# Optimization experiments

Hardware: AMD Instinct MI355X
Metric: run time of the kernel (lower is better)

Reference implementation:

```python
import jax, jax.numpy as jnp
import numpy as np

EPS = 1e-5  # BatchNorm eps


def _mlp(x, w1, b1, w2, b2, g, bt):
    # NRI MLP: elu(fc1) -> elu(fc2) -> batchnorm over all leading dims (training-mode batch stats)
    h = jax.nn.elu(x @ w1.T + b1)
    h = jax.nn.elu(h @ w2.T + b2)
    f = h.reshape(-1, h.shape[-1])
    mu = f.mean(0)
    var = f.var(0)  # biased, as in torch BN normalization
    return (h - mu) * jax.lax.rsqrt(var + EPS) * g + bt


def _gru(x, w_ih, w_hh, b_ih, b_hh):
    # x: [B, T, D] batch_first; torch GRU gate order (r, z, n)
    gi = jnp.einsum('btd,hd->bth', x, w_ih) + b_ih  # precompute input gates
    H = w_hh.shape[1]
    h0 = jnp.zeros((x.shape[0], H), x.dtype)

    def step(h, gi_t):
        gh = h @ w_hh.T + b_hh
        ir, iz, inn = jnp.split(gi_t, 3, -1)
        hr, hz, hn = jnp.split(gh, 3, -1)
        r = jax.nn.sigmoid(ir + hr)
        z = jax.nn.sigmoid(iz + hz)
        n = jnp.tanh(inn + r * hn)
        h_new = (1.0 - z) * n + z * h
        return h_new, h_new

    hT, ys = jax.lax.scan(step, h0, gi.transpose(1, 0, 2))
    return ys.transpose(1, 0, 2), hT


def _xavier(key, shape):
    std = np.sqrt(2.0 / (shape[0] + shape[1])).astype(np.float32)
    return jax.random.normal(key, shape, jnp.float32) * std


def setup_inputs() -> dict:
    key = jax.random.key(0)
    ks = iter(jax.random.split(key, 64))
    B, N, T, Fin, H, O = 8, 30, 100, 4, 128, 2
    inputs = jax.random.normal(next(ks), (B, N, T, Fin), jnp.float32)
    r, s = np.nonzero(1 - np.eye(N))  # fully connected, no self loops -> E = N*(N-1)
    eye = np.eye(N, dtype=np.float32)
    d = {
        'inputs': inputs,
        'rel_rec': jnp.asarray(eye[r]),
        'rel_send': jnp.asarray(eye[s]),
    }
    dims = {1: Fin, 2: 2 * H, 3: H, 4: 3 * H}
    for k in (1, 2, 3, 4):
        d[f'm{k}_w1'] = _xavier(next(ks), (H, dims[k]))
        d[f'm{k}_b1'] = jnp.full((H,), 0.1, jnp.float32)
        d[f'm{k}_w2'] = _xavier(next(ks), (H, H))
        d[f'm{k}_b2'] = jnp.full((H,), 0.1, jnp.float32)
        d[f'm{k}_g'] = jnp.ones((H,), jnp.float32)
        d[f'm{k}_bt'] = jnp.zeros((H,), jnp.float32)
    u = float(1.0 / np.sqrt(H))
    for p in ('gf', 'gr'):
        d[f'{p}_wih'] = jax.random.uniform(next(ks), (3 * H, H), jnp.float32, -u, u)
        d[f'{p}_whh'] = jax.random.uniform(next(ks), (3 * H, H), jnp.float32, -u, u)
        d[f'{p}_bih'] = jax.random.uniform(next(ks), (3 * H,), jnp.float32, -u, u)
        d[f'{p}_bhh'] = jax.random.uniform(next(ks), (3 * H,), jnp.float32, -u, u)
    d['pw'] = _xavier(next(ks), (O, H))
    d['pb'] = jnp.full((O,), 0.1, jnp.float32)
    d['ew'] = _xavier(next(ks), (O, 2 * H))
    d['eb'] = jnp.full((O,), 0.1, jnp.float32)
    return d


def reference(inputs, rel_rec, rel_send, m1_w1, m1_b1, m1_w2, m1_b2, m1_g, m1_bt, m2_w1, m2_b1, m2_w2, m2_b2, m2_g, m2_bt, m3_w1, m3_b1, m3_w2, m3_b2, m3_g, m3_bt, m4_w1, m4_b1, m4_w2, m4_b2, m4_g, m4_bt, gf_wih, gf_whh, gf_bih, gf_bhh, gr_wih, gr_whh, gr_bih, gr_bhh, pw, pb, ew, eb):
    N = rel_rec.shape[1]

    def node2edge(x):  # x: [B,N,T,H] -> [B,E,T,2H]
        snd = jnp.einsum('en,bnth->beth', rel_send, x)
        rcv = jnp.einsum('en,bnth->beth', rel_rec, x)
        return jnp.concatenate([snd, rcv], -1)

    def edge2node(x):  # x: [B,E,T,H] -> [B,N,T,H], mean-style normalization by N
        return jnp.einsum('en,beth->bnth', rel_rec, x) / N

    x = _mlp(inputs, m1_w1, m1_b1, m1_w2, m1_b2, m1_g, m1_bt)      # [B,N,T,H]
    x = node2edge(x)                                                # [B,E,T,2H]
    x = _mlp(x, m2_w1, m2_b1, m2_w2, m2_b2, m2_g, m2_bt)            # [B,E,T,H]
    x_skip = x
    x = edge2node(x)                                                # [B,N,T,H]
    x = _mlp(x, m3_w1, m3_b1, m3_w2, m3_b2, m3_g, m3_bt)
    x = node2edge(x)                                                # [B,E,T,2H]
    x = jnp.concatenate([x, x_skip], -1)                            # [B,E,T,3H]
    x = _mlp(x, m4_w1, m4_b1, m4_w2, m4_b2, m4_g, m4_bt)            # [B,E,T,H]

    B, E, T, H = x.shape
    xr = x.reshape(B * E, T, H)
    fwd_x, hT = _gru(xr, gf_wih, gf_whh, gf_bih, gf_bhh)
    rev_x, _ = _gru(xr[:, ::-1], gr_wih, gr_whh, gr_bih, gr_bhh)
    rev_x = rev_x[:, ::-1]

    prior = (fwd_x @ pw.T + pb).reshape(B, E, T, -1)
    comb = jnp.concatenate([fwd_x, rev_x], -1)
    enc = (comb @ ew.T + eb).reshape(B, E, T, -1)
    return prior, enc, hT[None]  # hT[None] matches torch GRU h_n [1, B*E, H]
```

## Files before the change

### kernel.cpp

```cpp
#include <hip/hip_runtime.h>
#include <math.h>

typedef float f32x4 __attribute__((ext_vector_type(4)));
typedef short bf16x8 __attribute__((ext_vector_type(8)));
typedef unsigned int uint32;
#define DEV static __device__ __forceinline__

constexpr int B_ = 8, N_ = 30, T_ = 100, FIN = 4, H_ = 128;
constexpr int E_ = N_*(N_-1);
constexpr int NSEQ = B_*E_;
constexpr int RN = B_*N_*T_;
constexpr int RE = B_*E_*T_;
constexpr int ET = E_*T_;
constexpr int NB_GRU = (NSEQ + 63)/64;

DEV float eluf(float x){ return x > 0.f ? x : __expf(x) - 1.f; }
DEV float sigmoidf(float x){ return 1.f/(1.f + __expf(-x)); }
DEV float tanhfast(float x){
  float cx = fminf(fmaxf(x, -20.f), 20.f);
  float e = __expf(2.f*cx);
  return (e - 1.f)/(e + 1.f);
}
DEV float dot4(f32x4 a, f32x4 b){ return a[0]*b[0] + a[1]*b[1] + a[2]*b[2] + a[3]*b[3]; }

DEV float bf2f(unsigned short u){ return __uint_as_float(((uint32)u) << 16); }
DEV uint32 f2bf_bits(float f){ uint32 b = __float_as_uint(f); return (b + 0x7FFFu + ((b >> 16) & 1u)) >> 16; }
DEV uint32 pack2(float lo, float hi){ return f2bf_bits(lo) | (f2bf_bits(hi) << 16); }

DEV bf16x8 cvt8(const float* __restrict__ p){
  f32x4 a = *(const f32x4*)p;
  f32x4 b = *(const f32x4*)(p+4);
  bf16x8 r;
  r[0]=(short)f2bf_bits(a[0]); r[1]=(short)f2bf_bits(a[1]);
  r[2]=(short)f2bf_bits(a[2]); r[3]=(short)f2bf_bits(a[3]);
  r[4]=(short)f2bf_bits(b[0]); r[5]=(short)f2bf_bits(b[1]);
  r[6]=(short)f2bf_bits(b[2]); r[7]=(short)f2bf_bits(b[3]);
  return r;
}

DEV void edge_decomp(int row, int& b, int& t, int& sn, int& ir)
{
  b = row / ET;
  int rem = row - b*ET;
  int e   = rem / T_;
  t = rem - e*T_;
  ir = e / (N_-1);
  int j = e - ir*(N_-1);
  sn = j + (j >= ir ? 1 : 0);
}

DEV int xcd_swizzle(int orig, int nwg)
{
  int q = nwg >> 3, r = nwg & 7;
  int xcd = orig & 7, j = orig >> 3;
  return (xcd < r ? xcd*(q+1) : r*(q+1) + (xcd-r)*q) + j;
}

__global__ __launch_bounds__(256)
void prep_weights(const float* __restrict__ w21, const float* __restrict__ w22,
                  const float* __restrict__ w41, const float* __restrict__ w42,
                  unsigned short* __restrict__ wbf)
{
  int idx = blockIdx.x*256 + threadIdx.x;
  if (idx >= 114688) return;
  float v;
  if (idx < 32768)      v = w21[idx];
  else if (idx < 49152) v = w22[idx - 32768];
  else if (idx < 98304) v = w41[idx - 49152];
  else                  v = w42[idx - 98304];
  wbf[idx] = (unsigned short)f2bf_bits(v);
}

template<int MODE, int DIN>
__global__ __launch_bounds__(256)
void mlp_fused(const float* __restrict__ src,
               const float* __restrict__ w1, const float* __restrict__ b1,
               const float* __restrict__ w2, const float* __restrict__ b2,
               float* __restrict__ out)
{
  constexpr int KC  = (DIN < 32) ? DIN : 32;
  constexpr int NCH = DIN / KC;
  __shared__ float As[KC][68];
  __shared__ float Ws[32][132];
  __shared__ float Hs[128][68];

  const int tid  = threadIdx.x;
  const int row0 = blockIdx.x * 64;
  const int tx = tid & 15, ty = tid >> 4;
  const int c0 = tx*8, r0 = ty*4;

  float acc[4][8];
  #pragma unroll
  for (int j=0;j<4;++j){
    #pragma unroll
    for (int i=0;i<8;++i) acc[j][i]=0.f;
  }

  for (int ch = 0; ch < NCH; ++ch) {
    for (int idx = tid; idx < 64*KC; idx += 256) {
      int r = idx / KC, k = idx % KC;
      As[k][r] = src[(size_t)(row0 + r)*DIN + ch*KC + k];
    }
    for (int idx = tid; idx < 128*KC; idx += 256) {
      int o = idx / KC, k = idx % KC;
      Ws[k][o] = w1[o*DIN + ch*KC + k];
    }
    __syncthreads();
    #pragma unroll
    for (int k = 0; k < KC; ++k) {
      f32x4 a  = *(const f32x4*)&As[k][r0];
      f32x4 wA = *(const f32x4*)&Ws[k][c0];
      f32x4 wB = *(const f32x4*)&Ws[k][c0+4];
      #pragma unroll
      for (int j=0;j<4;++j){
        #pragma unroll
        for (int i=0;i<4;++i){
          acc[j][i]   += a[j]*wA[i];
          acc[j][4+i] += a[j]*wB[i];
        }
      }
    }
    __syncthreads();
  }
  {
    #pragma unroll
    for (int i=0;i<8;++i){
      float bb = b1[c0+i];
      #pragma unroll
      for (int j=0;j<4;++j)
        Hs[c0+i][r0+j] = eluf(acc[j][i] + bb);
    }
  }
  __syncthreads();

  #pragma unroll
  for (int j=0;j<4;++j){
    #pragma unroll
    for (int i=0;i<8;++i) acc[j][i]=0.f;
  }

  for (int ch = 0; ch < 4; ++ch) {
    for (int idx = tid; idx < 128*32; idx += 256) {
      int o = idx >> 5, k = idx & 31;
      Ws[k][o] = w2[o*H_ + ch*32 + k];
    }
    __syncthreads();
    #pragma unroll
    for (int k = 0; k < 32; ++k) {
      f32x4 a  = *(const f32x4*)&Hs[ch*32 + k][r0];
      f32x4 wA = *(const f32x4*)&Ws[k][c0];
      f32x4 wB = *(const f32x4*)&Ws[k][c0+4];
      #pragma unroll
      for (int j=0;j<4;++j){
        #pragma unroll
        for (int i=0;i<4;++i){
          acc[j][i]   += a[j]*wA[i];
          acc[j][4+i] += a[j]*wB[i];
        }
      }
    }
    __syncthreads();
  }
  {
    #pragma unroll
    for (int j=0;j<4;++j){
      size_t base = (size_t)(row0 + r0 + j)*H_ + c0;
      #pragma unroll
      for (int i=0;i<8;++i) out[base+i] = eluf(acc[j][i] + b2[c0+i]);
    }
  }
}

__global__ __launch_bounds__(128)
void norm_to_bf16(const float* __restrict__ buf, int rows, const float* __restrict__ sums,
                  const float* __restrict__ g, const float* __restrict__ bt,
                  unsigned short* __restrict__ outbf)
{
  int c = threadIdx.x;
  float inv = 1.f/(float)rows;
  float mu  = sums[c]*inv;
  float var = sums[H_+c]*inv - mu*mu;
  float sc  = rsqrtf(var + 1e-5f)*g[c];
  float sh  = bt[c] - mu*sc;
  for (int r = blockIdx.x; r < rows; r += gridDim.x) {
    size_t idx = (size_t)r*H_ + c;
    outbf[idx] = (unsigned short)f2bf_bits(buf[idx]*sc + sh);
  }
}

__global__ __launch_bounds__(256, 2)
void mlp2_scatter(const unsigned short* __restrict__ x1bf,
                  const unsigned short* __restrict__ wbf,
                  const float* __restrict__ b21, const float* __restrict__ b22,
                  float* __restrict__ nodeB, float* __restrict__ stats2)
{
  __shared__ int srow[64], rrow[64];
  __shared__ __align__(16) char pool[17408];
  unsigned short* bufH = (unsigned short*)pool;
  float* red = (float*)pool;

  const int tid  = threadIdx.x;
  const int bid  = xcd_swizzle(blockIdx.x, gridDim.x);
  const int row0 = bid * 64;
  if (tid < 64) {
    int b,t,sn,ir; edge_decomp(row0 + tid, b, t, sn, ir);
    srow[tid] = (b*N_ + sn)*T_ + t;
    rrow[tid] = (b*N_ + ir)*T_ + t;
  }
  __syncthreads();

  const int lane = tid & 63;
  const int wv   = tid >> 6;
  const int c15  = lane & 15;
  const int k8   = (lane >> 4) * 8;
  const int g4   = (lane >> 4);
  const int colb = wv * 32;
  const unsigned short* W21 = wbf;
  const unsigned short* W22 = wbf + 32768;

  int sA[4], rA[4];
  #pragma unroll
  for (int rt=0;rt<4;++rt){ sA[rt] = srow[rt*16 + c15]; rA[rt] = rrow[rt*16 + c15]; }

  f32x4 C[2][4];

  #pragma unroll
  for (int ci=0;ci<2;++ci){
    float bb = b21[colb + ci*16 + c15];
    #pragma unroll
    for (int rt=0;rt<4;++rt) C[ci][rt] = (f32x4){bb,bb,bb,bb};
  }
  {
    bf16x8 Bf[2][8];
    #pragma unroll
    for (int ci=0;ci<2;++ci){
      #pragma unroll
      for (int kc=0;kc<8;++kc)
        Bf[ci][kc] = *(const bf16x8*)&W21[(size_t)(colb+ci*16+c15)*256 + kc*32 + k8];
    }
    #pragma unroll
    for (int kc=0;kc<8;++kc){
      bf16x8 A[4];
      #pragma unroll
      for (int rt=0;rt<4;++rt){
        int nrow = (kc<4) ? sA[rt] : rA[rt];
        A[rt] = *(const bf16x8*)&x1bf[(size_t)nrow*H_ + (kc&3)*32 + k8];
      }
      #pragma unroll
      for (int ci=0;ci<2;++ci){
        #pragma unroll
        for (int rt=0;rt<4;++rt)
          C[ci][rt] = __builtin_amdgcn_mfma_f32_16x16x32_bf16(A[rt], Bf[ci][kc], C[ci][rt], 0,0,0);
      }
    }
  }
  #pragma unroll
  for (int ci=0;ci<2;++ci){
    #pragma unroll
    for (int rt=0;rt<4;++rt){
      #pragma unroll
      for (int rr=0;rr<4;++rr){
        int row = rt*16 + g4*4 + rr;
        bufH[row*136 + colb + ci*16 + c15] = (unsigned short)f2bf_bits(eluf(C[ci][rt][rr]));
      }
    }
  }
  __syncthreads();

  #pragma unroll
  for (int ci=0;ci<2;++ci){
    float bb = b22[colb + ci*16 + c15];
    #pragma unroll
    for (int rt=0;rt<4;++rt) C[ci][rt] = (f32x4){bb,bb,bb,bb};
  }
  {
    bf16x8 Bf[2][4];
    #pragma unroll
    for (int ci=0;ci<2;++ci){
      #pragma unroll
      for (int kc=0;kc<4;++kc)
        Bf[ci][kc] = *(const bf16x8*)&W22[(size_t)(colb+ci*16+c15)*128 + kc*32 + k8];
    }
    #pragma unroll
    for (int kc=0;kc<4;++kc){
      bf16x8 A[4];
      #pragma unroll
      for (int rt=0;rt<4;++rt)
        A[rt] = *(const bf16x8*)&bufH[(rt*16+c15)*136 + kc*32 + k8];
      #pragma unroll
      for (int ci=0;ci<2;++ci){
        #pragma unroll
        for (int rt=0;rt<4;++rt)
          C[ci][rt] = __builtin_amdgcn_mfma_f32_16x16x32_bf16(A[rt], Bf[ci][kc], C[ci][rt], 0,0,0);
      }
    }
  }

  float s1l[2], s2l[2];
  #pragma unroll
  for (int ci=0;ci<2;++ci){ s1l[ci]=0.f; s2l[ci]=0.f; }
  #pragma unroll
  for (int ci=0;ci<2;++ci){
    int col = colb + ci*16 + c15;
    #pragma unroll
    for (int rt=0;rt<4;++rt){
      #pragma unroll
      for (int rr=0;rr<4;++rr){
        int row = rt*16 + g4*4 + rr;
        float v = eluf(C[ci][rt][rr]);
        atomicAdd(&nodeB[(size_t)rrow[row]*H_ + col], v);
        s1l[ci] += v; s2l[ci] += v*v;
      }
    }
  }
  __syncthreads();
  #pragma unroll
  for (int ci=0;ci<2;++ci){
    int col = colb + ci*16 + c15;
    red[col*4 + g4]       = s1l[ci];
    red[512 + col*4 + g4] = s2l[ci];
  }
  __syncthreads();
  if (tid < 128) {
    float s=0.f, q=0.f;
    #pragma unroll
    for (int u=0;u<4;++u){ s += red[tid*4+u]; q += red[512 + tid*4+u]; }
    atomicAdd(&stats2[tid], s);
    atomicAdd(&stats2[128+tid], q);
  }
}

__global__ __launch_bounds__(256, 2)
void mlp24_fused(const unsigned short* __restrict__ x1bf, const unsigned short* __restrict__ x3bf,
                 const float* __restrict__ aff2, const unsigned short* __restrict__ wbf,
                 const float* __restrict__ b21, const float* __restrict__ b22,
                 const float* __restrict__ b41, const float* __restrict__ b42,
                 unsigned short* __restrict__ x4pre, float* __restrict__ stats4)
{
  __shared__ int srow[64], rrow[64];
  __shared__ __align__(16) char pool[34816];
  unsigned short* bufH = (unsigned short*)pool;
  unsigned short* bufX = (unsigned short*)(pool + 17408);
  float* red = (float*)pool;

  const int tid  = threadIdx.x;
  const int bid  = xcd_swizzle(blockIdx.x, gridDim.x);
  const int row0 = bid * 64;
  if (tid < 64) {
    int b,t,sn,ir; edge_decomp(row0 + tid, b, t, sn, ir);
    srow[tid] = (b*N_ + sn)*T_ + t;
    rrow[tid] = (b*N_ + ir)*T_ + t;
  }
  __syncthreads();

  const int lane = tid & 63;
  const int wv   = tid >> 6;
  const int c15  = lane & 15;
  const int k8   = (lane >> 4) * 8;
  const int g4   = (lane >> 4);
  const int colb = wv * 32;
  const unsigned short* W21 = wbf;
  const unsigned short* W22 = wbf + 32768;
  const unsigned short* W41 = wbf + 49152;
  const unsigned short* W42 = wbf + 98304;

  int sA[4], rA[4];
  #pragma unroll
  for (int rt=0;rt<4;++rt){ sA[rt] = srow[rt*16 + c15]; rA[rt] = rrow[rt*16 + c15]; }

  f32x4 C[2][4];

  #pragma unroll
  for (int ci=0;ci<2;++ci){
    float bb = b21[colb + ci*16 + c15];
    #pragma unroll
    for (int rt=0;rt<4;++rt) C[ci][rt] = (f32x4){bb,bb,bb,bb};
  }
  {
    bf16x8 Bf[2][8];
    #pragma unroll
    for (int ci=0;ci<2;++ci){
      #pragma unroll
      for (int kc=0;kc<8;++kc)
        Bf[ci][kc] = *(const bf16x8*)&W21[(size_t)(colb+ci*16+c15)*256 + kc*32 + k8];
    }
    #pragma unroll
    for (int kc=0;kc<8;++kc){
      bf16x8 A[4];
      #pragma unroll
      for (int rt=0;rt<4;++rt){
        int nrow = (kc<4) ? sA[rt] : rA[rt];
        A[rt] = *(const bf16x8*)&x1bf[(size_t)nrow*H_ + (kc&3)*32 + k8];
      }
      #pragma unroll
      for (int ci=0;ci<2;++ci){
        #pragma unroll
        for (int rt=0;rt<4;++rt)
          C[ci][rt] = __builtin_amdgcn_mfma_f32_16x16x32_bf16(A[rt], Bf[ci][kc], C[ci][rt], 0,0,0);
      }
    }
  }
  #pragma unroll
  for (int ci=0;ci<2;++ci){
    #pragma unroll
    for (int rt=0;rt<4;++rt){
      #pragma unroll
      for (int rr=0;rr<4;++rr){
        int row = rt*16 + g4*4 + rr;
        bufH[row*136 + colb + ci*16 + c15] = (unsigned short)f2bf_bits(eluf(C[ci][rt][rr]));
      }
    }
  }
  __syncthreads();

  #pragma unroll
  for (int ci=0;ci<2;++ci){
    float bb = b22[colb + ci*16 + c15];
    #pragma unroll
    for (int rt=0;rt<4;++rt) C[ci][rt] = (f32x4){bb,bb,bb,bb};
  }
  {
    bf16x8 Bf[2][4];
    #pragma unroll
    for (int ci=0;ci<2;++ci){
      #pragma unroll
      for (int kc=0;kc<4;++kc)
        Bf[ci][kc] = *(const bf16x8*)&W22[(size_t)(colb+ci*16+c15)*128 + kc*32 + k8];
    }
    #pragma unroll
    for (int kc=0;kc<4;++kc){
      bf16x8 A[4];
      #pragma unroll
      for (int rt=0;rt<4;++rt)
        A[rt] = *(const bf16x8*)&bufH[(rt*16+c15)*136 + kc*32 + k8];
      #pragma unroll
      for (int ci=0;ci<2;++ci){
        #pragma unroll
        for (int rt=0;rt<4;++rt)
          C[ci][rt] = __builtin_amdgcn_mfma_f32_16x16x32_bf16(A[rt], Bf[ci][kc], C[ci][rt], 0,0,0);
      }
    }
  }
  #pragma unroll
  for (int ci=0;ci<2;++ci){
    int col = colb + ci*16 + c15;
    float sc = aff2[col], sh = aff2[128+col];
    #pragma unroll
    for (int rt=0;rt<4;++rt){
      #pragma unroll
      for (int rr=0;rr<4;++rr){
        int row = rt*16 + g4*4 + rr;
        bufX[row*136 + col] = (unsigned short)f2bf_bits(eluf(C[ci][rt][rr])*sc + sh);
      }
    }
  }
  __syncthreads();

  #pragma unroll
  for (int ci=0;ci<2;++ci){
    float bb = b41[colb + ci*16 + c15];
    #pragma unroll
    for (int rt=0;rt<4;++rt) C[ci][rt] = (f32x4){bb,bb,bb,bb};
  }
  {
    bf16x8 Bf[2][6];
    #pragma unroll
    for (int ci=0;ci<2;++ci){
      #pragma unroll
      for (int kc=0;kc<6;++kc)
        Bf[ci][kc] = *(const bf16x8*)&W41[(size_t)(colb+ci*16+c15)*384 + kc*32 + k8];
    }
    #pragma unroll
    for (int kc=0;kc<6;++kc){
      bf16x8 A[4];
      #pragma unroll
      for (int rt=0;rt<4;++rt){
        if (kc < 4) A[rt] = *(const bf16x8*)&x3bf[(size_t)sA[rt]*H_ + kc*32 + k8];
        else        A[rt] = *(const bf16x8*)&x3bf[(size_t)rA[rt]*H_ + (kc-4)*32 + k8];
      }
      #pragma unroll
      for (int ci=0;ci<2;++ci){
        #pragma unroll
        for (int rt=0;rt<4;++rt)
          C[ci][rt] = __builtin_amdgcn_mfma_f32_16x16x32_bf16(A[rt], Bf[ci][kc], C[ci][rt], 0,0,0);
      }
    }
    #pragma unroll
    for (int ci=0;ci<2;++ci){
      #pragma unroll
      for (int kc=0;kc<6;++kc)
        Bf[ci][kc] = *(const bf16x8*)&W41[(size_t)(colb+ci*16+c15)*384 + (kc+6)*32 + k8];
    }
    #pragma unroll
    for (int kc=6;kc<12;++kc){
      bf16x8 A[4];
      #pragma unroll
      for (int rt=0;rt<4;++rt){
        if (kc < 8) A[rt] = *(const bf16x8*)&x3bf[(size_t)rA[rt]*H_ + (kc-4)*32 + k8];
        else        A[rt] = *(const bf16x8*)&bufX[(rt*16+c15)*136 + (kc-8)*32 + k8];
      }
      #pragma unroll
      for (int ci=0;ci<2;++ci){
        #pragma unroll
        for (int rt=0;rt<4;++rt)
          C[ci][rt] = __builtin_amdgcn_mfma_f32_16x16x32_bf16(A[rt], Bf[ci][kc-6], C[ci][rt], 0,0,0);
      }
    }
  }
  __syncthreads();
  #pragma unroll
  for (int ci=0;ci<2;++ci){
    #pragma unroll
    for (int rt=0;rt<4;++rt){
      #pragma unroll
      for (int rr=0;rr<4;++rr){
        int row = rt*16 + g4*4 + rr;
        bufH[row*136 + colb + ci*16 + c15] = (unsigned short)f2bf_bits(eluf(C[ci][rt][rr]));
      }
    }
  }
  __syncthreads();

  #pragma unroll
  for (int ci=0;ci<2;++ci){
    float bb = b42[colb + ci*16 + c15];
    #pragma unroll
    for (int rt=0;rt<4;++rt) C[ci][rt] = (f32x4){bb,bb,bb,bb};
  }
  {
    bf16x8 Bf[2][4];
    #pragma unroll
    for (int ci=0;ci<2;++ci){
      #pragma unroll
      for (int kc=0;kc<4;++kc)
        Bf[ci][kc] = *(const bf16x8*)&W42[(size_t)(colb+ci*16+c15)*128 + kc*32 + k8];
    }
    #pragma unroll
    for (int kc=0;kc<4;++kc){
      bf16x8 A[4];
      #pragma unroll
      for (int rt=0;rt<4;++rt)
        A[rt] = *(const bf16x8*)&bufH[(rt*16+c15)*136 + kc*32 + k8];
      #pragma unroll
      for (int ci=0;ci<2;++ci){
        #pragma unroll
        for (int rt=0;rt<4;++rt)
          C[ci][rt] = __builtin_amdgcn_mfma_f32_16x16x32_bf16(A[rt], Bf[ci][kc], C[ci][rt], 0,0,0);
      }
    }
  }
  float s1l[2], s2l[2];
  #pragma unroll
  for (int ci=0;ci<2;++ci){ s1l[ci]=0.f; s2l[ci]=0.f; }
  #pragma unroll
  for (int ci=0;ci<2;++ci){
    int col = colb + ci*16 + c15;
    #pragma unroll
    for (int rt=0;rt<4;++rt){
      #pragma unroll
      for (int rr=0;rr<4;++rr){
        int row = rt*16 + g4*4 + rr;
        float v = eluf(C[ci][rt][rr]);
        x4pre[(size_t)(row0 + row)*H_ + col] = (unsigned short)f2bf_bits(v);
        s1l[ci] += v; s2l[ci] += v*v;
      }
    }
  }
  __syncthreads();
  #pragma unroll
  for (int ci=0;ci<2;++ci){
    int col = colb + ci*16 + c15;
    red[col*4 + g4]       = s1l[ci];
    red[512 + col*4 + g4] = s2l[ci];
  }
  __syncthreads();
  if (tid < 128) {
    float s=0.f, q=0.f;
    #pragma unroll
    for (int u=0;u<4;++u){ s += red[tid*4+u]; q += red[512 + tid*4+u]; }
    atomicAdd(&stats4[tid], s);
    atomicAdd(&stats4[128+tid], q);
  }
}

__global__ __launch_bounds__(128)
void stats_kernel(const float* __restrict__ buf, int rows, float* __restrict__ sums)
{
  int c = threadIdx.x;
  float s = 0.f, s2 = 0.f;
  for (int r = blockIdx.x; r < rows; r += gridDim.x) {
    float v = buf[(size_t)r*H_ + c];
    s += v; s2 += v*v;
  }
  atomicAdd(&sums[c], s);
  atomicAdd(&sums[H_ + c], s2);
}

__global__ __launch_bounds__(128)
void finalize_aff(const float* __restrict__ sums, const float* __restrict__ g,
                  const float* __restrict__ bt, float* __restrict__ aff, int rows)
{
  int c = threadIdx.x;
  float inv = 1.f/(float)rows;
  float mu  = sums[c]*inv;
  float var = sums[H_+c]*inv - mu*mu;
  float sc  = rsqrtf(var + 1e-5f)*g[c];
  aff[c]      = sc;
  aff[H_ + c] = bt[c] - mu*sc;
}

__global__ __launch_bounds__(256)
void e2n_finalize(float* __restrict__ nodeB, const float* __restrict__ aff2)
{
  int idx = blockIdx.x*256 + threadIdx.x;
  if (idx >= RN*H_) return;
  int c = idx & 127;
  nodeB[idx] = (nodeB[idx]*aff2[c] + (float)(N_-1)*aff2[128+c]) * (1.f/(float)N_);
}

__global__ __launch_bounds__(512, 1)
void gru_kernel(const unsigned short* __restrict__ x4pre, const float* __restrict__ aff4,
                const float* __restrict__ wihf, const float* __restrict__ whhf,
                const float* __restrict__ bihf, const float* __restrict__ bhhf,
                const float* __restrict__ wihr, const float* __restrict__ whhr,
                const float* __restrict__ bihr, const float* __restrict__ bhhr,
                const float* __restrict__ pw, const float* __restrict__ pb,
                const float* __restrict__ ew, const float* __restrict__ eb,
                float* __restrict__ out_prior, float* __restrict__ out_enc,
                float* __restrict__ out_hT)
{
  __shared__ __align__(16) unsigned short As[64*264];
  __shared__ __align__(16) float hs[64*132];
  __shared__ float sc4[128], sh4[128];

  const int tid  = threadIdx.x;
  const int dir  = blockIdx.x / NB_GRU;
  const int blk  = blockIdx.x % NB_GRU;
  const int seq0 = blk * 64;
  const int lane = tid & 63;
  const int wv   = __builtin_amdgcn_readfirstlane(tid >> 6);
  const int j0   = wv * 16;
  const int c15  = lane & 15;
  const int k8g  = (lane >> 4) * 8;

  const float* wih = dir ? wihr : wihf;
  const float* whh = dir ? whhr : whhf;
  const float* bih = dir ? bihr : bihf;
  const float* bhh = dir ? bhhr : bhhf;

  bf16x8 Br[8], Bz[8], Bi[4], Bn[4];
  #pragma unroll
  for (int kt=0; kt<8; ++kt){
    const float* sr = (kt<4) ? (wih + (size_t)(j0+c15)*H_ + kt*32 + k8g)
                             : (whh + (size_t)(j0+c15)*H_ + (kt-4)*32 + k8g);
    Br[kt] = cvt8(sr);
    const float* sz = (kt<4) ? (wih + (size_t)(128+j0+c15)*H_ + kt*32 + k8g)
                             : (whh + (size_t)(128+j0+c15)*H_ + (kt-4)*32 + k8g);
    Bz[kt] = cvt8(sz);
  }
  #pragma unroll
  for (int kt=0; kt<4; ++kt){
    Bi[kt] = cvt8(wih + (size_t)(256+j0+c15)*H_ + kt*32 + k8g);
    Bn[kt] = cvt8(whh + (size_t)(256+j0+c15)*H_ + kt*32 + k8g);
  }
  const float bR = bih[j0+c15]     + bhh[j0+c15];
  const float bZ = bih[128+j0+c15] + bhh[128+j0+c15];
  const float bI = bih[256+j0+c15];
  const float bN = bhh[256+j0+c15];

  for (int i = tid; i < 64*264; i += 512) As[i] = 0;
  for (int i = tid; i < 64*132; i += 512) hs[i] = 0.f;
  if (tid < 128) { sc4[tid] = aff4[tid]; sh4[tid] = aff4[H_+tid]; }
  float hreg[16];
  #pragma unroll
  for (int i=0;i<16;++i) hreg[i] = 0.f;
  __syncthreads();

  const int ss = tid >> 3;
  const int cc = (tid & 7) * 16;
  const int qq = seq0 + ss;

  for (int step = 0; step < T_; ++step) {
    const int t = dir ? (T_-1-step) : step;

    {
      float xv16[16];
      if (qq < NSEQ) {
        const uint32* gp = (const uint32*)(x4pre + ((size_t)qq*T_ + t)*H_ + cc);
        uint32 w[8];
        #pragma unroll
        for (int u=0;u<8;++u) w[u] = gp[u];
        #pragma unroll
        for (int u=0;u<8;++u) {
          float lo = __uint_as_float(w[u] << 16);
          float hi = __uint_as_float(w[u] & 0xFFFF0000u);
          xv16[2*u]   = lo*sc4[cc+2*u]   + sh4[cc+2*u];
          xv16[2*u+1] = hi*sc4[cc+2*u+1] + sh4[cc+2*u+1];
        }
      } else {
        #pragma unroll
        for (int u=0;u<16;++u) xv16[u] = 0.f;
      }
      uint32* xp = (uint32*)(As + ss*264 + cc);
      #pragma unroll
      for (int u=0;u<8;++u) xp[u] = pack2(xv16[2*u], xv16[2*u+1]);
    }
    __syncthreads();

    f32x4 Cr[4], Cz[4], Ci[4], Cn[4];
    #pragma unroll
    for (int rt=0;rt<4;++rt){
      Cr[rt] = (f32x4){bR,bR,bR,bR};
      Cz[rt] = (f32x4){bZ,bZ,bZ,bZ};
      Ci[rt] = (f32x4){bI,bI,bI,bI};
      Cn[rt] = (f32x4){bN,bN,bN,bN};
    }
    #pragma unroll
    for (int kt=0; kt<8; ++kt){
      bf16x8 a0 = *(const bf16x8*)&As[(size_t)( 0+c15)*264 + kt*32 + k8g];
      bf16x8 a1 = *(const bf16x8*)&As[(size_t)(16+c15)*264 + kt*32 + k8g];
      bf16x8 a2 = *(const bf16x8*)&As[(size_t)(32+c15)*264 + kt*32 + k8g];
      bf16x8 a3 = *(const bf16x8*)&As[(size_t)(48+c15)*264 + kt*32 + k8g];
      Cr[0] = __builtin_amdgcn_mfma_f32_16x16x32_bf16(a0, Br[kt], Cr[0], 0,0,0);
      Cr[1] = __builtin_amdgcn_mfma_f32_16x16x32_bf16(a1, Br[kt], Cr[1], 0,0,0);
      Cr[2] = __builtin_amdgcn_mfma_f32_16x16x32_bf16(a2, Br[kt], Cr[2], 0,0,0);
      Cr[3] = __builtin_amdgcn_mfma_f32_16x16x32_bf16(a3, Br[kt], Cr[3], 0,0,0);
      Cz[0] = __builtin_amdgcn_mfma_f32_16x16x32_bf16(a0, Bz[kt], Cz[0], 0,0,0);
      Cz[1] = __builtin_amdgcn_mfma_f32_16x16x32_bf16(a1, Bz[kt], Cz[1], 0,0,0);
      Cz[2] = __builtin_amdgcn_mfma_f32_16x16x32_bf16(a2, Bz[kt], Cz[2], 0,0,0);
      Cz[3] = __builtin_amdgcn_mfma_f32_16x16x32_bf16(a3, Bz[kt], Cz[3], 0,0,0);
      if (kt < 4) {
        Ci[0] = __builtin_amdgcn_mfma_f32_16x16x32_bf16(a0, Bi[kt], Ci[0], 0,0,0);
        Ci[1] = __builtin_amdgcn_mfma_f32_16x16x32_bf16(a1, Bi[kt], Ci[1], 0,0,0);
        Ci[2] = __builtin_amdgcn_mfma_f32_16x16x32_bf16(a2, Bi[kt], Ci[2], 0,0,0);
        Ci[3] = __builtin_amdgcn_mfma_f32_16x16x32_bf16(a3, Bi[kt], Ci[3], 0,0,0);
      } else {
        Cn[0] = __builtin_amdgcn_mfma_f32_16x16x32_bf16(a0, Bn[kt-4], Cn[0], 0,0,0);
        Cn[1] = __builtin_amdgcn_mfma_f32_16x16x32_bf16(a1, Bn[kt-4], Cn[1], 0,0,0);
        Cn[2] = __builtin_amdgcn_mfma_f32_16x16x32_bf16(a2, Bn[kt-4], Cn[2], 0,0,0);
        Cn[3] = __builtin_amdgcn_mfma_f32_16x16x32_bf16(a3, Bn[kt-4], Cn[3], 0,0,0);
      }
    }
    __syncthreads();

    #pragma unroll
    for (int rt=0;rt<4;++rt){
      #pragma unroll
      for (int rr=0;rr<4;++rr){
        float r_ = sigmoidf(Cr[rt][rr]);
        float z_ = sigmoidf(Cz[rt][rr]);
        float n_ = tanhfast(Ci[rt][rr] + r_*Cn[rt][rr]);
        float hn = (1.f - z_)*n_ + z_*hreg[rt*4+rr];
        hreg[rt*4+rr] = hn;
        int row = rt*16 + (lane>>4)*4 + rr;
        As[(size_t)row*264 + 128 + j0 + c15] = (unsigned short)f2bf_bits(hn);
        hs[row*132 + j0 + c15] = hn;
      }
    }
    __syncthreads();

    if (qq < NSEQ) {
      const f32x4* hrow = (const f32x4*)(hs + ss*132 + cc);
      f32x4 h0=hrow[0], h1=hrow[1], h2=hrow[2], h3=hrow[3];
      size_t obase = ((size_t)qq*T_ + t)*2;
      if (dir == 0) {
        const f32x4* pw0 = (const f32x4*)(pw + cc);
        const f32x4* pw1 = (const f32x4*)(pw + H_ + cc);
        const f32x4* ew0 = (const f32x4*)(ew + cc);
        const f32x4* ew1 = (const f32x4*)(ew + 2*H_ + cc);
        float p0 = dot4(pw0[0],h0)+dot4(pw0[1],h1)+dot4(pw0[2],h2)+dot4(pw0[3],h3);
        float p1 = dot4(pw1[0],h0)+dot4(pw1[1],h1)+dot4(pw1[2],h2)+dot4(pw1[3],h3);
        float e0 = dot4(ew0[0],h0)+dot4(ew0[1],h1)+dot4(ew0[2],h2)+dot4(ew0[3],h3);
        float e1 = dot4(ew1[0],h0)+dot4(ew1[1],h1)+dot4(ew1[2],h2)+dot4(ew1[3],h3);
        #pragma unroll
        for (int m=1;m<8;m<<=1){
          p0 += __shfl_xor(p0,m); p1 += __shfl_xor(p1,m);
          e0 += __shfl_xor(e0,m); e1 += __shfl_xor(e1,m);
        }
        if ((tid & 7) == 0) {
          out_prior[obase]   = p0 + pb[0];
          out_prior[obase+1] = p1 + pb[1];
          atomicAdd(&out_enc[obase],   e0);
          atomicAdd(&out_enc[obase+1], e1);
        }
      } else {
        const f32x4* ew0 = (const f32x4*)(ew + H_ + cc);
        const f32x4* ew1 = (const f32x4*)(ew + 2*H_ + H_ + cc);
        float e0 = dot4(ew0[0],h0)+dot4(ew0[1],h1)+dot4(ew0[2],h2)+dot4(ew0[3],h3);
        float e1 = dot4(ew1[0],h0)+dot4(ew1[1],h1)+dot4(ew1[2],h2)+dot4(ew1[3],h3);
        #pragma unroll
        for (int m=1;m<8;m<<=1){
          e0 += __shfl_xor(e0,m); e1 += __shfl_xor(e1,m);
        }
        if ((tid & 7) == 0) {
          atomicAdd(&out_enc[obase],   e0 + eb[0]);
          atomicAdd(&out_enc[obase+1], e1 + eb[1]);
        }
      }
    }
  }

  if (dir == 0) {
    __syncthreads();
    for (int idx = tid; idx < 64*H_; idx += 512) {
      int s = idx >> 7, c = idx & 127;
      int q = seq0 + s;
      if (q < NSEQ) out_hT[(size_t)q*H_ + c] = hs[s*132 + c];
    }
  }
}

__global__ void ws_report(float* out, float v){ out[0] = v; }

extern "C" void kernel_launch(void* const* d_in, const int* in_sizes, int n_in,
                              void* d_out, int out_size, void* d_ws, size_t ws_size,
                              hipStream_t stream)
{
  (void)in_sizes; (void)n_in; (void)out_size;
  const float* inputs = (const float*)d_in[0];
  const float* m1_w1 = (const float*)d_in[3];  const float* m1_b1 = (const float*)d_in[4];
  const float* m1_w2 = (const float*)d_in[5];  const float* m1_b2 = (const float*)d_in[6];
  const float* m1_g  = (const float*)d_in[7];  const float* m1_bt = (const float*)d_in[8];
  const float* m2_w1 = (const float*)d_in[9];  const float* m2_b1 = (const float*)d_in[10];
  const float* m2_w2 = (const float*)d_in[11]; const float* m2_b2 = (const float*)d_in[12];
  const float* m2_g  = (const float*)d_in[13]; const float* m2_bt = (const float*)d_in[14];
  const float* m3_w1 = (const float*)d_in[15]; const float* m3_b1 = (const float*)d_in[16];
  const float* m3_w2 = (const float*)d_in[17]; const float* m3_b2 = (const float*)d_in[18];
  const float* m3_g  = (const float*)d_in[19]; const float* m3_bt = (const float*)d_in[20];
  const float* m4_w1 = (const float*)d_in[21]; const float* m4_b1 = (const float*)d_in[22];
  const float* m4_w2 = (const float*)d_in[23]; const float* m4_b2 = (const float*)d_in[24];
  const float* m4_g  = (const float*)d_in[25]; const float* m4_bt = (const float*)d_in[26];
  const float* gf_wih = (const float*)d_in[27]; const float* gf_whh = (const float*)d_in[28];
  const float* gf_bih = (const float*)d_in[29]; const float* gf_bhh = (const float*)d_in[30];
  const float* gr_wih = (const float*)d_in[31]; const float* gr_whh = (const float*)d_in[32];
  const float* gr_bih = (const float*)d_in[33]; const float* gr_bhh = (const float*)d_in[34];
  const float* pw = (const float*)d_in[35]; const float* pb = (const float*)d_in[36];
  const float* ew = (const float*)d_in[37]; const float* eb = (const float*)d_in[38];

  float* out       = (float*)d_out;
  float* out_prior = out;
  float* out_enc   = out + (size_t)RE*2;
  float* out_hT    = out + (size_t)RE*4;

  size_t x4elems = (size_t)RE*H_;
  size_t nodeElems = (size_t)RN*H_;
  unsigned short* x4pre = (unsigned short*)d_ws;
  float* nodeA = (float*)(x4pre + x4elems);
  float* nodeB = nodeA + nodeElems;
  float* nodeC = nodeB + nodeElems;
  float* stats = nodeC + nodeElems;
  float* aff   = stats + 1024;
  unsigned short* wbf  = (unsigned short*)(aff + 512);
  unsigned short* x1bf = wbf + 114688;
  unsigned short* x3bf = (unsigned short*)nodeA;
  size_t need = (size_t)((char*)(x1bf + nodeElems) - (char*)d_ws);
  if (ws_size < need) {
    ws_report<<<1, 1, 0, stream>>>(out_prior, (float)ws_size);
    return;
  }

  (void)hipMemsetAsync(stats, 0, 1024*sizeof(float), stream);
  (void)hipMemsetAsync(nodeB, 0, nodeElems*sizeof(float), stream);
  (void)hipMemsetAsync(out_enc, 0, (size_t)RE*2*sizeof(float), stream);

  prep_weights<<<448, 256, 0, stream>>>(m2_w1, m2_w2, m4_w1, m4_w2, wbf);

  mlp_fused<0, FIN><<<RN/64, 256, 0, stream>>>(inputs, m1_w1, m1_b1, m1_w2, m1_b2, nodeA);
  stats_kernel<<<512, 128, 0, stream>>>(nodeA, RN, stats + 0);
  norm_to_bf16<<<512, 128, 0, stream>>>(nodeA, RN, stats + 0, m1_g, m1_bt, x1bf);

  mlp2_scatter<<<RE/64, 256, 0, stream>>>(x1bf, wbf, m2_b1, m2_b2, nodeB, stats + 256);
  finalize_aff<<<1, 128, 0, stream>>>(stats + 256, m2_g, m2_bt, aff + 0, RE);
  e2n_finalize<<<(RN*H_ + 255)/256, 256, 0, stream>>>(nodeB, aff + 0);

  mlp_fused<2, H_><<<RN/64, 256, 0, stream>>>(nodeB, m3_w1, m3_b1, m3_w2, m3_b2, nodeC);
  stats_kernel<<<512, 128, 0, stream>>>(nodeC, RN, stats + 512);
  norm_to_bf16<<<512, 128, 0, stream>>>(nodeC, RN, stats + 512, m3_g, m3_bt, x3bf);

  mlp24_fused<<<RE/64, 256, 0, stream>>>(x1bf, x3bf, aff + 0, wbf,
      m2_b1, m2_b2, m4_b1, m4_b2, x4pre, stats + 768);
  finalize_aff<<<1, 128, 0, stream>>>(stats + 768, m4_g, m4_bt, aff + 256, RE);

  gru_kernel<<<2*NB_GRU, 512, 0, stream>>>(x4pre, aff + 256,
      gf_wih, gf_whh, gf_bih, gf_bhh,
      gr_wih, gr_whh, gr_bih, gr_bhh,
      pw, pb, ew, eb, out_prior, out_enc, out_hT);
}
```

Baseline: 2.082 ms.

## Pre-normalize GRU input and prefetch next timestep into registers

New measurement: 2.016 ms. -3.1%, faster.

```diff
diff --git a/kernel.cpp b/kernel.cpp
--- a/kernel.cpp
+++ b/kernel.cpp
@@ -186,6 +186,28 @@
     size_t idx = (size_t)r*H_ + c;
     outbf[idx] = (unsigned short)f2bf_bits(buf[idx]*sc + sh);
   }
+}
+
+__global__ __launch_bounds__(256)
+void apply_aff4(unsigned short* __restrict__ x4, const float* __restrict__ aff)
+{
+  size_t idx = ((size_t)blockIdx.x*256 + threadIdx.x)*8;
+  int c = (int)(idx & 127);
+  uint32* p = (uint32*)(x4 + idx);
+  uint32 win[4];
+  #pragma unroll
+  for (int u=0;u<4;++u) win[u] = p[u];
+  uint32 o[4];
+  #pragma unroll
+  for (int u=0;u<4;++u){
+    float lo = __uint_as_float(win[u] << 16);
+    float hi = __uint_as_float(win[u] & 0xFFFF0000u);
+    float a = lo*aff[c+2*u]   + aff[128+c+2*u];
+    float b = hi*aff[c+2*u+1] + aff[128+c+2*u+1];
+    o[u] = pack2(a, b);
+  }
+  #pragma unroll
+  for (int u=0;u<4;++u) p[u] = o[u];
 }
 
 __global__ __launch_bounds__(256, 2)
@@ -619,7 +641,7 @@
 }
 
 __global__ __launch_bounds__(512, 1)
-void gru_kernel(const unsigned short* __restrict__ x4pre, const float* __restrict__ aff4,
+void gru_kernel(const unsigned short* __restrict__ x4n,
                 const float* __restrict__ wihf, const float* __restrict__ whhf,
                 const float* __restrict__ bihf, const float* __restrict__ bhhf,
                 const float* __restrict__ wihr, const float* __restrict__ whhr,
@@ -631,7 +653,8 @@
 {
   __shared__ __align__(16) unsigned short As[64*264];
   __shared__ __align__(16) float hs[64*132];
-  __shared__ float sc4[128], sh4[128];
+  __shared__ float pws[256];
+  __shared__ float ews[512];
 
   const int tid  = threadIdx.x;
   const int dir  = blockIdx.x / NB_GRU;
@@ -667,45 +690,52 @@
   const float bZ = bih[128+j0+c15] + bhh[128+j0+c15];
   const float bI = bih[256+j0+c15];
   const float bN = bhh[256+j0+c15];
+  const float pb0 = pb[0], pb1 = pb[1], eb0 = eb[0], eb1 = eb[1];
 
   for (int i = tid; i < 64*264; i += 512) As[i] = 0;
   for (int i = tid; i < 64*132; i += 512) hs[i] = 0.f;
-  if (tid < 128) { sc4[tid] = aff4[tid]; sh4[tid] = aff4[H_+tid]; }
+  for (int i = tid; i < 256; i += 512) pws[i] = pw[i];
+  for (int i = tid; i < 512; i += 512) ews[i] = ew[i];
   float hreg[16];
   #pragma unroll
   for (int i=0;i<16;++i) hreg[i] = 0.f;
-  __syncthreads();
 
   const int ss = tid >> 3;
   const int cc = (tid & 7) * 16;
   const int qq = seq0 + ss;
 
+  uint32 xw[8];
+  {
+    int t0 = dir ? (T_-1) : 0;
+    if (qq < NSEQ) {
+      const uint32* gp = (const uint32*)(x4n + ((size_t)qq*T_ + t0)*H_ + cc);
+      #pragma unroll
+      for (int u=0;u<8;++u) xw[u] = gp[u];
+    } else {
+      #pragma unroll
+      for (int u=0;u<8;++u) xw[u] = 0;
+    }
+  }
+  __syncthreads();
+
   for (int step = 0; step < T_; ++step) {
     const int t = dir ? (T_-1-step) : step;
 
     {
-      float xv16[16];
+      uint32* xp = (uint32*)(As + ss*264 + cc);
+      #pragma unroll
+      for (int u=0;u<8;++u) xp[u] = xw[u];
+    }
+    __syncthreads();
+
+    if (step + 1 < T_) {
+      int tn = dir ? (T_-2-step) : (step+1);
       if (qq < NSEQ) {
-        const uint32* gp = (const uint32*)(x4pre + ((size_t)qq*T_ + t)*H_ + cc);
-        uint32 w[8];
-        #pragma unroll
-        for (int u=0;u<8;++u) w[u] = gp[u];
-        #pragma unroll
-        for (int u=0;u<8;++u) {
-          float lo = __uint_as_float(w[u] << 16);
-          float hi = __uint_as_float(w[u] & 0xFFFF0000u);
-          xv16[2*u]   = lo*sc4[cc+2*u]   + sh4[cc+2*u];
-          xv16[2*u+1] = hi*sc4[cc+2*u+1] + sh4[cc+2*u+1];
-        }
-      } else {
-        #pragma unroll
-        for (int u=0;u<16;++u) xv16[u] = 0.f;
-      }
-      uint32* xp = (uint32*)(As + ss*264 + cc);
-      #pragma unroll
-      for (int u=0;u<8;++u) xp[u] = pack2(xv16[2*u], xv16[2*u+1]);
-    }
-    __syncthreads();
+        const uint32* gp = (const uint32*)(x4n + ((size_t)qq*T_ + tn)*H_ + cc);
+        #pragma unroll
+        for (int u=0;u<8;++u) xw[u] = gp[u];
+      }
+    }
 
     f32x4 Cr[4], Cz[4], Ci[4], Cn[4];
     #pragma unroll
@@ -764,10 +794,10 @@
       f32x4 h0=hrow[0], h1=hrow[1], h2=hrow[2], h3=hrow[3];
       size_t obase = ((size_t)qq*T_ + t)*2;
       if (dir == 0) {
-        const f32x4* pw0 = (const f32x4*)(pw + cc);
-        const f32x4* pw1 = (const f32x4*)(pw + H_ + cc);
-        const f32x4* ew0 = (const f32x4*)(ew + cc);
-        const f32x4* ew1 = (const f32x4*)(ew + 2*H_ + cc);
+        const f32x4* pw0 = (const f32x4*)(pws + cc);
+        const f32x4* pw1 = (const f32x4*)(pws + H_ + cc);
+        const f32x4* ew0 = (const f32x4*)(ews + cc);
+        const f32x4* ew1 = (const f32x4*)(ews + 2*H_ + cc);
         float p0 = dot4(pw0[0],h0)+dot4(pw0[1],h1)+dot4(pw0[2],h2)+dot4(pw0[3],h3);
         float p1 = dot4(pw1[0],h0)+dot4(pw1[1],h1)+dot4(pw1[2],h2)+dot4(pw1[3],h3);
         float e0 = dot4(ew0[0],h0)+dot4(ew0[1],h1)+dot4(ew0[2],h2)+dot4(ew0[3],h3);
@@ -778,14 +808,14 @@
           e0 += __shfl_xor(e0,m); e1 += __shfl_xor(e1,m);
         }
         if ((tid & 7) == 0) {
-          out_prior[obase]   = p0 + pb[0];
-          out_prior[obase+1] = p1 + pb[1];
+          out_prior[obase]   = p0 + pb0;
+          out_prior[obase+1] = p1 + pb1;
           atomicAdd(&out_enc[obase],   e0);
           atomicAdd(&out_enc[obase+1], e1);
         }
       } else {
-        const f32x4* ew0 = (const f32x4*)(ew + H_ + cc);
-        const f32x4* ew1 = (const f32x4*)(ew + 2*H_ + H_ + cc);
+        const f32x4* ew0 = (const f32x4*)(ews + H_ + cc);
+        const f32x4* ew1 = (const f32x4*)(ews + 2*H_ + H_ + cc);
         float e0 = dot4(ew0[0],h0)+dot4(ew0[1],h1)+dot4(ew0[2],h2)+dot4(ew0[3],h3);
         float e1 = dot4(ew1[0],h0)+dot4(ew1[1],h1)+dot4(ew1[2],h2)+dot4(ew1[3],h3);
         #pragma unroll
@@ -793,8 +823,8 @@
           e0 += __shfl_xor(e0,m); e1 += __shfl_xor(e1,m);
         }
         if ((tid & 7) == 0) {
-          atomicAdd(&out_enc[obase],   e0 + eb[0]);
-          atomicAdd(&out_enc[obase+1], e1 + eb[1]);
+          atomicAdd(&out_enc[obase],   e0 + eb0);
+          atomicAdd(&out_enc[obase+1], e1 + eb1);
         }
       }
     }
@@ -881,7 +911,9 @@
       m2_b1, m2_b2, m4_b1, m4_b2, x4pre, stats + 768);
   finalize_aff<<<1, 128, 0, stream>>>(stats + 768, m4_g, m4_bt, aff + 256, RE);
 
-  gru_kernel<<<2*NB_GRU, 512, 0, stream>>>(x4pre, aff + 256,
+  apply_aff4<<<(int)(x4elems/(256*8)), 256, 0, stream>>>(x4pre, aff + 256);
+
+  gru_kernel<<<2*NB_GRU, 512, 0, stream>>>(x4pre,
       gf_wih, gf_whh, gf_bih, gf_bhh,
       gr_wih, gr_whh, gr_bih, gr_bhh,
       pw, pb, ew, eb, out_prior, out_enc, out_hT);
```
